# Kernel optimization log

Hardware: AMD Instinct MI355X
Metric: run time of the kernel (lower is better)

## Reference

```python
import jax, jax.numpy as jnp
import numpy as np

WINDOWS = ((0, 4), (2, 6), (4, 8))
N_CLASSES = 64
EPS = 1e-12  # F.normalize eps


def setup_inputs() -> dict:
    key = jax.random.key(0)
    k1, k2 = jax.random.split(key)
    S, Q, T, D = 256, 4096, 8, 1024
    support_features = jax.random.normal(k1, (S, T, D), dtype=jnp.float32)
    target_features = jax.random.normal(k2, (Q, T, D), dtype=jnp.float32)
    support_labels = jnp.arange(S, dtype=jnp.int32) % N_CLASSES  # 4 shots per class, sorted-unique order
    logit_scale = jnp.array(0.0, dtype=jnp.float32)
    fusion_logits = jnp.zeros((3,), dtype=jnp.float32)
    return {
        'support_features': support_features,
        'target_features': target_features,
        'support_labels': support_labels,
        'logit_scale': logit_scale,
        'fusion_logits': fusion_logits,
    }


def _l2norm(x):
    n = jnp.sqrt(jnp.sum(x * x, axis=-1, keepdims=True))
    return x / jnp.maximum(n, EPS)


def _pairwise_dist(query_seq, support_seq):
    # query_seq: [Q, Tq, D], support_seq: [K, Ts, D] -> 1 - cosine sim [Q, K, Tq, Ts]
    sim = jnp.einsum('qtd,ksd->qkts', _l2norm(query_seq), _l2norm(support_seq))
    return 1.0 - sim


def _bi_mhm(dists):
    # dists: [Q, K, Tq, Ts]
    return dists.min(axis=3).sum(axis=2) + dists.min(axis=2).sum(axis=2)


def _segments(features):
    # features: [N, T, D] -> [N, n_windows, D] (mean over each window)
    return jnp.stack([features[:, s:e, :].mean(axis=1) for s, e in WINDOWS], axis=1)


def _prototypes(features, labels):
    # scatter-mean over class labels; features: [S, ...], labels: [S]
    sums = jax.ops.segment_sum(features, labels, num_segments=N_CLASSES)
    counts = jax.ops.segment_sum(jnp.ones((features.shape[0],), features.dtype), labels,
                                 num_segments=N_CLASSES)
    return sums / counts[:, None, None]


def reference(support_features, target_features, support_labels, logit_scale, fusion_logits):
    # global (frame-level) bidirectional min-sum chamfer distance to class prototypes
    support_proto = _prototypes(support_features, support_labels)          # [K, T, D]
    global_dist = _bi_mhm(_pairwise_dist(target_features, support_proto))  # [Q, K]

    # segment-level distances
    support_segments = _segments(support_features)                          # [S, 3, D]
    target_segments = _segments(target_features)                            # [Q, 3, D]
    support_seg_proto = _prototypes(support_segments, support_labels)       # [K, 3, D]
    seg_dist = _pairwise_dist(target_segments, support_seg_proto)           # [Q, K, 3, 3]
    seg_q2s = seg_dist.min(axis=3).sum(axis=2)
    seg_s2q = seg_dist.min(axis=2).sum(axis=2)

    fusion = jax.nn.softmax(fusion_logits)
    fused = (fusion[0] * global_dist + fusion[1] * seg_s2q + fusion[2] * seg_q2s)
    fused = fused * jnp.exp(logit_scale)
    return (-fused, -global_dist, -seg_s2q, -seg_q2s)
```

## Files before the change

### kernel.cpp

```cpp
#include <hip/hip_runtime.h>
#include <stdint.h>

typedef unsigned short u16;
typedef short short8 __attribute__((ext_vector_type(8)));
typedef float floatx4 __attribute__((ext_vector_type(4)));

#define KDIM 1024
#define QN   4096
#define KCLS 64
#define QK   (QN * KCLS)


__device__ __forceinline__ u16 f2bf(float x) {
  union { float f; uint32_t u; } un; un.f = x;
  uint32_t u = un.u;
  u += 0x7FFFu + ((u >> 16) & 1u);
  return (u16)(u >> 16);
}

struct alignas(16) F4 { float x, y, z, w; };
struct alignas(8)  U16x4 { u16 a, b, c, d; };

__device__ __forceinline__ float block_sum(float v) {
  __shared__ float sb[4];
  #pragma unroll
  for (int m = 1; m < 64; m <<= 1) v += __shfl_xor(v, m);
  int tid = threadIdx.x;
  if ((tid & 63) == 0) sb[tid >> 6] = v;
  __syncthreads();
  return sb[0] + sb[1] + sb[2] + sb[3];
}

__device__ __forceinline__ void norm_store(float v0, float v1, float v2, float v3,
                                           u16* __restrict__ dst_row, int tid) {
  float ss = block_sum(v0*v0 + v1*v1 + v2*v2 + v3*v3);
  float inv = 1.0f / fmaxf(sqrtf(ss), 1e-12f);
  U16x4 o; o.a = f2bf(v0*inv); o.b = f2bf(v1*inv); o.c = f2bf(v2*inv); o.d = f2bf(v3*inv);
  *(U16x4*)(dst_row + tid*4) = o;
}


__global__ __launch_bounds__(256) void proto_kernel(const float* __restrict__ S,
                                                    u16* __restrict__ Bg) {
  int b = blockIdx.x, tid = threadIdx.x;
  int k = b >> 3, t = b & 7;
  float v0 = 0.f, v1 = 0.f, v2 = 0.f, v3 = 0.f;
  #pragma unroll
  for (int s = 0; s < 4; ++s) {
    const F4 x = *(const F4*)(S + (size_t)(((s*64 + k)*8 + t))*1024 + tid*4);
    v0 += x.x; v1 += x.y; v2 += x.z; v3 += x.w;
  }
  norm_store(v0*0.25f, v1*0.25f, v2*0.25f, v3*0.25f, Bg + (size_t)b*1024, tid);
}

__global__ __launch_bounds__(256) void segproto_kernel(const float* __restrict__ S,
                                                       u16* __restrict__ Bs) {
  int b = blockIdx.x, tid = threadIdx.x;
  int k = b >> 2, w = b & 3;
  if (w == 3) { U16x4 z; z.a = z.b = z.c = z.d = 0; *(U16x4*)(Bs + (size_t)b*1024 + tid*4) = z; return; }
  int t0 = w * 2;
  float v0 = 0.f, v1 = 0.f, v2 = 0.f, v3 = 0.f;
  #pragma unroll
  for (int s = 0; s < 4; ++s)
    #pragma unroll
    for (int f = 0; f < 4; ++f) {
      const F4 x = *(const F4*)(S + (size_t)(((s*64 + k)*8 + t0 + f))*1024 + tid*4);
      v0 += x.x; v1 += x.y; v2 += x.z; v3 += x.w;
    }
  const float c = 1.0f / 16.0f;
  norm_store(v0*c, v1*c, v2*c, v3*c, Bs + (size_t)b*1024, tid);
}

__global__ __launch_bounds__(256) void tnorm_kernel(const float* __restrict__ T,
                                                    u16* __restrict__ Ag) {
  int b = blockIdx.x, tid = threadIdx.x;
  const F4 x = *(const F4*)(T + (size_t)b*1024 + tid*4);
  norm_store(x.x, x.y, x.z, x.w, Ag + (size_t)b*1024, tid);
}

__global__ __launch_bounds__(256) void tseg_kernel(const float* __restrict__ T,
                                                   u16* __restrict__ As) {
  int b = blockIdx.x, tid = threadIdx.x;
  int q = b >> 2, w = b & 3;
  if (w == 3) { U16x4 z; z.a = z.b = z.c = z.d = 0; *(U16x4*)(As + (size_t)b*1024 + tid*4) = z; return; }
  int t0 = w * 2;
  float v0 = 0.f, v1 = 0.f, v2 = 0.f, v3 = 0.f;
  #pragma unroll
  for (int f = 0; f < 4; ++f) {
    const F4 x = *(const F4*)(T + (size_t)(q*8 + t0 + f)*1024 + tid*4);
    v0 += x.x; v1 += x.y; v2 += x.z; v3 += x.w;
  }
  norm_store(v0*0.25f, v1*0.25f, v2*0.25f, v3*0.25f, As + (size_t)b*1024, tid);
}


__device__ __forceinline__ void load_lds16(const u16* g, u16* l) {
  __builtin_amdgcn_global_load_lds((__attribute__((address_space(1))) void*)(g),
                                   (__attribute__((address_space(3))) void*)(l),
                                   16, 0, 0);
}

template <int MODE>
__global__ __launch_bounds__(256) void gemm_kernel(const u16* __restrict__ A,
                                                   const u16* __restrict__ B,
                                                   float* __restrict__ out_a,
                                                   float* __restrict__ out_b) {
  __shared__ __align__(16) u16 At[128 * 64];
  __shared__ __align__(16) u16 Bt[128 * 64];

  const int tid  = threadIdx.x;
  const int lane = tid & 63;
  const int wave = tid >> 6;
  const int wm = wave >> 1, wn = wave & 1;
  const int rowA0 = blockIdx.y * 128;
  const int rowB0 = blockIdx.x * 128;

  floatx4 acc[4][4] = {};

  const int srow = lane >> 3;
  const int scol = ((lane & 7) ^ srow) * 8;

  for (int kb = 0; kb < KDIM; kb += 64) {
    __syncthreads();
    #pragma unroll
    for (int it = 0; it < 4; ++it) {
      const int c = wave * 4 + it;
      load_lds16(A + (size_t)(rowA0 + c*8 + srow) * KDIM + kb + scol, &At[c * 512]);
      load_lds16(B + (size_t)(rowB0 + c*8 + srow) * KDIM + kb + scol, &Bt[c * 512]);
    }
    __syncthreads();
    #pragma unroll
    for (int kk = 0; kk < 2; ++kk) {
      const int kc0 = kk * 4 + (lane >> 4);
      short8 af[4], bf[4];
      #pragma unroll
      for (int i = 0; i < 4; ++i) {
        const int row = wm*64 + i*16 + (lane & 15);
        af[i] = *(const short8*)&At[row*64 + ((kc0 ^ (row & 7)) * 8)];
        const int col = wn*64 + i*16 + (lane & 15);
        bf[i] = *(const short8*)&Bt[col*64 + ((kc0 ^ (col & 7)) * 8)];
      }
      #pragma unroll
      for (int i = 0; i < 4; ++i)
        #pragma unroll
        for (int j = 0; j < 4; ++j)
          acc[i][j] = __builtin_amdgcn_mfma_f32_16x16x32_bf16(af[i], bf[j], acc[i][j], 0, 0, 0);
    }
  }

  if (MODE == 0) {
    const int qBase = blockIdx.y * 16 + wm * 8;
    const int kBase = blockIdx.x * 16 + wn * 8;
    #pragma unroll
    for (int i = 0; i < 4; ++i) {
      #pragma unroll
      for (int j = 0; j < 4; ++j) {
        floatx4 c = acc[i][j];
        float rs = 0.f;
        #pragma unroll
        for (int r = 0; r < 4; ++r) {
          float x = c[r];
          x = fmaxf(x, __shfl_xor(x, 1));
          x = fmaxf(x, __shfl_xor(x, 2));
          x = fmaxf(x, __shfl_xor(x, 4));
          rs += x;
        }
        rs += __shfl_xor(rs, 16);
        float cm = fmaxf(fmaxf(c[0], c[1]), fmaxf(c[2], c[3]));
        cm = fmaxf(cm, __shfl_xor(cm, 16));
        float cs = cm;
        cs += __shfl_xor(cs, 1);
        cs += __shfl_xor(cs, 2);
        cs += __shfl_xor(cs, 4);
        const float tot = rs + cs - 16.0f;
        if ((lane & 23) == 0) {
          const int a = lane >> 5, bb = (lane >> 3) & 1;
          out_a[(size_t)(qBase + i*2 + a) * KCLS + (kBase + j*2 + bb)] = tot;
        }
      }
    }
  } else {
    const int qBase = blockIdx.y * 32 + wm * 16;
    const int kBase = blockIdx.x * 32 + wn * 16;
    const int cv = lane & 3;
    #pragma unroll
    for (int i = 0; i < 4; ++i) {
      #pragma unroll
      for (int j = 0; j < 4; ++j) {
        floatx4 c = acc[i][j];
        float rsum = 0.f;
        #pragma unroll
        for (int r = 0; r < 3; ++r) {
          float x = (cv == 3) ? -3.0e38f : c[r];
          x = fmaxf(x, __shfl_xor(x, 1));
          x = fmaxf(x, __shfl_xor(x, 2));
          rsum += x;
        }
        float cm = fmaxf(fmaxf(c[0], c[1]), c[2]);
        float y = (cv == 3) ? 0.f : cm;
        y += __shfl_xor(y, 1);
        y += __shfl_xor(y, 2);
        if (cv == 0) {
          const int q = qBase + i*4 + (lane >> 4);
          const int k = kBase + j*4 + ((lane >> 2) & 3);
          out_a[(size_t)q * KCLS + k] = y - 3.0f;
          out_b[(size_t)q * KCLS + k] = rsum - 3.0f;
        }
      }
    }
  }
}

__global__ __launch_bounds__(256) void fuse_kernel(const float* __restrict__ fl,
                                                   const float* __restrict__ ls,
                                                   const float* __restrict__ g,
                                                   const float* __restrict__ s2q,
                                                   const float* __restrict__ q2s,
                                                   float* __restrict__ out) {
  const int i = blockIdx.x * 256 + threadIdx.x;
  const float f0 = fl[0], f1 = fl[1], f2 = fl[2];
  const float m = fmaxf(f0, fmaxf(f1, f2));
  const float e0 = expf(f0 - m), e1 = expf(f1 - m), e2 = expf(f2 - m);
  const float sc = expf(ls[0]) / (e0 + e1 + e2);
  out[i] = sc * (e0 * g[i] + e1 * s2q[i] + e2 * q2s[i]);
}


extern "C" void kernel_launch(void* const* d_in, const int* in_sizes, int n_in,
                              void* d_out, int out_size, void* d_ws, size_t ws_size,
                              hipStream_t stream) {
  (void)in_sizes; (void)n_in; (void)out_size; (void)ws_size;
  const float* S  = (const float*)d_in[0];
  const float* T  = (const float*)d_in[1];
  const float* ls = (const float*)d_in[3];
  const float* fl = (const float*)d_in[4];

  float* outF   = (float*)d_out;
  float* outG   = outF + QK;
  float* outS2Q = outF + 2 * (size_t)QK;
  float* outQ2S = outF + 3 * (size_t)QK;

  u16* Ag = (u16*)d_ws;
  u16* As = Ag + (size_t)32768 * 1024;
  u16* Bg = As + (size_t)16384 * 1024;
  u16* Bs = Bg + (size_t)512 * 1024;

  tnorm_kernel   <<<32768, 256, 0, stream>>>(T, Ag);
  tseg_kernel    <<<16384, 256, 0, stream>>>(T, As);
  proto_kernel   <<<512,   256, 0, stream>>>(S, Bg);
  segproto_kernel<<<256,   256, 0, stream>>>(S, Bs);

  gemm_kernel<0><<<dim3(4, 256), 256, 0, stream>>>(Ag, Bg, outG, outG);
  gemm_kernel<1><<<dim3(2, 128), 256, 0, stream>>>(As, Bs, outS2Q, outQ2S);

  fuse_kernel<<<QK / 256, 256, 0, stream>>>(fl, ls, outG, outS2Q, outQ2S, outF);
}
```

Measured before the change: 318.7 us.

## Fuse preprocessing kernels and fold final fusion into segment GEMM epilogue

Merges the four normalization/segment kernels into two per-row kernels that read each target sample's eight frames once and emit both frame-level and segment-level normalized bf16 rows, with all eleven norms reduced together. Support prototypes are likewise built once per class. The separate fuse kernel is removed, and the segment GEMM epilogue computes the fused output directly by reading the global distance. The aim is to cut redundant global reads of the target tensor and the extra launches and elementwise pass. The trade-offs are more registers in the prep kernels and the segment GEMM depending on the global GEMM having finished writing outG, which stream ordering guarantees.

```diff
diff --git a/kernel.cpp b/kernel.cpp
--- a/kernel.cpp
+++ b/kernel.cpp
@@ -21,76 +21,133 @@
 struct alignas(16) F4 { float x, y, z, w; };
 struct alignas(8)  U16x4 { u16 a, b, c, d; };
 
-__device__ __forceinline__ float block_sum(float v) {
-  __shared__ float sb[4];
-  #pragma unroll
-  for (int m = 1; m < 64; m <<= 1) v += __shfl_xor(v, m);
-  int tid = threadIdx.x;
-  if ((tid & 63) == 0) sb[tid >> 6] = v;
+__device__ __forceinline__ float dot4(const F4& a, const F4& b) {
+  return a.x*b.x + a.y*b.y + a.z*b.z + a.w*b.w;
+}
+
+
+__device__ __forceinline__ void reduce11(float (&ss)[11], float (&tot)[11],
+                                         float (*sb)[12], int lane, int wave) {
+  #pragma unroll
+  for (int v = 0; v < 11; ++v) {
+    float x = ss[v];
+    #pragma unroll
+    for (int m = 1; m < 64; m <<= 1) x += __shfl_xor(x, m);
+    ss[v] = x;
+  }
+  if (lane == 0) {
+    #pragma unroll
+    for (int v = 0; v < 11; ++v) sb[wave][v] = ss[v];
+  }
   __syncthreads();
-  return sb[0] + sb[1] + sb[2] + sb[3];
-}
-
-__device__ __forceinline__ void norm_store(float v0, float v1, float v2, float v3,
-                                           u16* __restrict__ dst_row, int tid) {
-  float ss = block_sum(v0*v0 + v1*v1 + v2*v2 + v3*v3);
-  float inv = 1.0f / fmaxf(sqrtf(ss), 1e-12f);
-  U16x4 o; o.a = f2bf(v0*inv); o.b = f2bf(v1*inv); o.c = f2bf(v2*inv); o.d = f2bf(v3*inv);
-  *(U16x4*)(dst_row + tid*4) = o;
-}
-
-
-__global__ __launch_bounds__(256) void proto_kernel(const float* __restrict__ S,
-                                                    u16* __restrict__ Bg) {
-  int b = blockIdx.x, tid = threadIdx.x;
-  int k = b >> 3, t = b & 7;
-  float v0 = 0.f, v1 = 0.f, v2 = 0.f, v3 = 0.f;
-  #pragma unroll
-  for (int s = 0; s < 4; ++s) {
-    const F4 x = *(const F4*)(S + (size_t)(((s*64 + k)*8 + t))*1024 + tid*4);
-    v0 += x.x; v1 += x.y; v2 += x.z; v3 += x.w;
-  }
-  norm_store(v0*0.25f, v1*0.25f, v2*0.25f, v3*0.25f, Bg + (size_t)b*1024, tid);
-}
-
-__global__ __launch_bounds__(256) void segproto_kernel(const float* __restrict__ S,
-                                                       u16* __restrict__ Bs) {
-  int b = blockIdx.x, tid = threadIdx.x;
-  int k = b >> 2, w = b & 3;
-  if (w == 3) { U16x4 z; z.a = z.b = z.c = z.d = 0; *(U16x4*)(Bs + (size_t)b*1024 + tid*4) = z; return; }
-  int t0 = w * 2;
-  float v0 = 0.f, v1 = 0.f, v2 = 0.f, v3 = 0.f;
+  #pragma unroll
+  for (int v = 0; v < 11; ++v)
+    tot[v] = sb[0][v] + sb[1][v] + sb[2][v] + sb[3][v];
+}
+
+__device__ __forceinline__ float inv_norm(float ss) {
+  return 1.0f / fmaxf(sqrtf(ss), 1e-12f);
+}
+
+__global__ __launch_bounds__(256) void prep_T(const float* __restrict__ T,
+                                              u16* __restrict__ Ag,
+                                              u16* __restrict__ As) {
+  __shared__ float sb[4][12];
+  const int q = blockIdx.x, tid = threadIdx.x;
+  const int lane = tid & 63, wave = tid >> 6;
+
+  F4 x[8];
+  #pragma unroll
+  for (int t = 0; t < 8; ++t)
+    x[t] = *(const F4*)(T + (size_t)(q*8 + t)*1024 + tid*4);
+
+  float ss[11], tot[11];
+  #pragma unroll
+  for (int t = 0; t < 8; ++t) ss[t] = dot4(x[t], x[t]);
+  #pragma unroll
+  for (int w = 0; w < 3; ++w) {
+    F4 y;
+    y.x = (x[2*w].x + x[2*w+1].x + x[2*w+2].x + x[2*w+3].x) * 0.25f;
+    y.y = (x[2*w].y + x[2*w+1].y + x[2*w+2].y + x[2*w+3].y) * 0.25f;
+    y.z = (x[2*w].z + x[2*w+1].z + x[2*w+2].z + x[2*w+3].z) * 0.25f;
+    y.w = (x[2*w].w + x[2*w+1].w + x[2*w+2].w + x[2*w+3].w) * 0.25f;
+    ss[8+w] = dot4(y, y);
+  }
+  reduce11(ss, tot, sb, lane, wave);
+
+  #pragma unroll
+  for (int t = 0; t < 8; ++t) {
+    const float inv = inv_norm(tot[t]);
+    U16x4 o; o.a = f2bf(x[t].x*inv); o.b = f2bf(x[t].y*inv);
+    o.c = f2bf(x[t].z*inv); o.d = f2bf(x[t].w*inv);
+    *(U16x4*)(Ag + (size_t)(q*8 + t)*1024 + tid*4) = o;
+  }
+  #pragma unroll
+  for (int w = 0; w < 3; ++w) {
+    const float inv = inv_norm(tot[8+w]) * 0.25f;
+    F4 y;
+    y.x = (x[2*w].x + x[2*w+1].x + x[2*w+2].x + x[2*w+3].x) * inv;
+    y.y = (x[2*w].y + x[2*w+1].y + x[2*w+2].y + x[2*w+3].y) * inv;
+    y.z = (x[2*w].z + x[2*w+1].z + x[2*w+2].z + x[2*w+3].z) * inv;
+    y.w = (x[2*w].w + x[2*w+1].w + x[2*w+2].w + x[2*w+3].w) * inv;
+    U16x4 o; o.a = f2bf(y.x); o.b = f2bf(y.y); o.c = f2bf(y.z); o.d = f2bf(y.w);
+    *(U16x4*)(As + (size_t)(q*4 + w)*1024 + tid*4) = o;
+  }
+  U16x4 z; z.a = z.b = z.c = z.d = 0;
+  *(U16x4*)(As + (size_t)(q*4 + 3)*1024 + tid*4) = z;
+}
+
+__global__ __launch_bounds__(256) void prep_S(const float* __restrict__ S,
+                                              u16* __restrict__ Bg,
+                                              u16* __restrict__ Bs) {
+  __shared__ float sb[4][12];
+  const int k = blockIdx.x, tid = threadIdx.x;
+  const int lane = tid & 63, wave = tid >> 6;
+
+  F4 p[8];
+  #pragma unroll
+  for (int t = 0; t < 8; ++t) { p[t].x = 0.f; p[t].y = 0.f; p[t].z = 0.f; p[t].w = 0.f; }
   #pragma unroll
   for (int s = 0; s < 4; ++s)
     #pragma unroll
-    for (int f = 0; f < 4; ++f) {
-      const F4 x = *(const F4*)(S + (size_t)(((s*64 + k)*8 + t0 + f))*1024 + tid*4);
-      v0 += x.x; v1 += x.y; v2 += x.z; v3 += x.w;
-    }
-  const float c = 1.0f / 16.0f;
-  norm_store(v0*c, v1*c, v2*c, v3*c, Bs + (size_t)b*1024, tid);
-}
-
-__global__ __launch_bounds__(256) void tnorm_kernel(const float* __restrict__ T,
-                                                    u16* __restrict__ Ag) {
-  int b = blockIdx.x, tid = threadIdx.x;
-  const F4 x = *(const F4*)(T + (size_t)b*1024 + tid*4);
-  norm_store(x.x, x.y, x.z, x.w, Ag + (size_t)b*1024, tid);
-}
-
-__global__ __launch_bounds__(256) void tseg_kernel(const float* __restrict__ T,
-                                                   u16* __restrict__ As) {
-  int b = blockIdx.x, tid = threadIdx.x;
-  int q = b >> 2, w = b & 3;
-  if (w == 3) { U16x4 z; z.a = z.b = z.c = z.d = 0; *(U16x4*)(As + (size_t)b*1024 + tid*4) = z; return; }
-  int t0 = w * 2;
-  float v0 = 0.f, v1 = 0.f, v2 = 0.f, v3 = 0.f;
-  #pragma unroll
-  for (int f = 0; f < 4; ++f) {
-    const F4 x = *(const F4*)(T + (size_t)(q*8 + t0 + f)*1024 + tid*4);
-    v0 += x.x; v1 += x.y; v2 += x.z; v3 += x.w;
-  }
-  norm_store(v0*0.25f, v1*0.25f, v2*0.25f, v3*0.25f, As + (size_t)b*1024, tid);
+    for (int t = 0; t < 8; ++t) {
+      const F4 v = *(const F4*)(S + (size_t)(((s*64 + k)*8 + t))*1024 + tid*4);
+      p[t].x += v.x; p[t].y += v.y; p[t].z += v.z; p[t].w += v.w;
+    }
+  float ss[11], tot[11];
+  #pragma unroll
+  for (int t = 0; t < 8; ++t) ss[t] = dot4(p[t], p[t]) * (0.25f * 0.25f);
+  #pragma unroll
+  for (int w = 0; w < 3; ++w) {
+    F4 y;
+    y.x = (p[2*w].x + p[2*w+1].x + p[2*w+2].x + p[2*w+3].x) * 0.0625f;
+    y.y = (p[2*w].y + p[2*w+1].y + p[2*w+2].y + p[2*w+3].y) * 0.0625f;
+    y.z = (p[2*w].z + p[2*w+1].z + p[2*w+2].z + p[2*w+3].z) * 0.0625f;
+    y.w = (p[2*w].w + p[2*w+1].w + p[2*w+2].w + p[2*w+3].w) * 0.0625f;
+    ss[8+w] = dot4(y, y);
+  }
+  reduce11(ss, tot, sb, lane, wave);
+
+  #pragma unroll
+  for (int t = 0; t < 8; ++t) {
+    const float inv = inv_norm(tot[t]) * 0.25f;
+    U16x4 o; o.a = f2bf(p[t].x*inv); o.b = f2bf(p[t].y*inv);
+    o.c = f2bf(p[t].z*inv); o.d = f2bf(p[t].w*inv);
+    *(U16x4*)(Bg + (size_t)(k*8 + t)*1024 + tid*4) = o;
+  }
+  #pragma unroll
+  for (int w = 0; w < 3; ++w) {
+    const float inv = inv_norm(tot[8+w]) * 0.0625f;
+    F4 y;
+    y.x = (p[2*w].x + p[2*w+1].x + p[2*w+2].x + p[2*w+3].x) * inv;
+    y.y = (p[2*w].y + p[2*w+1].y + p[2*w+2].y + p[2*w+3].y) * inv;
+    y.z = (p[2*w].z + p[2*w+1].z + p[2*w+2].z + p[2*w+3].z) * inv;
+    y.w = (p[2*w].w + p[2*w+1].w + p[2*w+2].w + p[2*w+3].w) * inv;
+    U16x4 o; o.a = f2bf(y.x); o.b = f2bf(y.y); o.c = f2bf(y.z); o.d = f2bf(y.w);
+    *(U16x4*)(Bs + (size_t)(k*4 + w)*1024 + tid*4) = o;
+  }
+  U16x4 z; z.a = z.b = z.c = z.d = 0;
+  *(U16x4*)(Bs + (size_t)(k*4 + 3)*1024 + tid*4) = z;
 }
 
 
@@ -104,7 +161,11 @@
 __global__ __launch_bounds__(256) void gemm_kernel(const u16* __restrict__ A,
                                                    const u16* __restrict__ B,
                                                    float* __restrict__ out_a,
-                                                   float* __restrict__ out_b) {
+                                                   float* __restrict__ out_b,
+                                                   const float* __restrict__ outG,
+                                                   float* __restrict__ out_f,
+                                                   const float* __restrict__ fl,
+                                                   const float* __restrict__ ls) {
   __shared__ __align__(16) u16 At[128 * 64];
   __shared__ __align__(16) u16 Bt[128 * 64];
 
@@ -180,6 +241,10 @@
       }
     }
   } else {
+    const float f0 = fl[0], f1 = fl[1], f2 = fl[2];
+    const float mx = fmaxf(f0, fmaxf(f1, f2));
+    const float e0 = __expf(f0 - mx), e1 = __expf(f1 - mx), e2 = __expf(f2 - mx);
+    const float sc = __expf(ls[0]) / (e0 + e1 + e2);
     const int qBase = blockIdx.y * 32 + wm * 16;
     const int kBase = blockIdx.x * 32 + wn * 16;
     const int cv = lane & 3;
@@ -203,26 +268,16 @@
         if (cv == 0) {
           const int q = qBase + i*4 + (lane >> 4);
           const int k = kBase + j*4 + ((lane >> 2) & 3);
-          out_a[(size_t)q * KCLS + k] = y - 3.0f;
-          out_b[(size_t)q * KCLS + k] = rsum - 3.0f;
+          const size_t idx = (size_t)q * KCLS + k;
+          const float s2q = y - 3.0f;
+          const float q2s = rsum - 3.0f;
+          out_a[idx] = s2q;
+          out_b[idx] = q2s;
+          out_f[idx] = sc * (e0 * outG[idx] + e1 * s2q + e2 * q2s);
         }
       }
     }
   }
-}
-
-__global__ __launch_bounds__(256) void fuse_kernel(const float* __restrict__ fl,
-                                                   const float* __restrict__ ls,
-                                                   const float* __restrict__ g,
-                                                   const float* __restrict__ s2q,
-                                                   const float* __restrict__ q2s,
-                                                   float* __restrict__ out) {
-  const int i = blockIdx.x * 256 + threadIdx.x;
-  const float f0 = fl[0], f1 = fl[1], f2 = fl[2];
-  const float m = fmaxf(f0, fmaxf(f1, f2));
-  const float e0 = expf(f0 - m), e1 = expf(f1 - m), e2 = expf(f2 - m);
-  const float sc = expf(ls[0]) / (e0 + e1 + e2);
-  out[i] = sc * (e0 * g[i] + e1 * s2q[i] + e2 * q2s[i]);
 }
 
 
@@ -245,13 +300,9 @@
   u16* Bg = As + (size_t)16384 * 1024;
   u16* Bs = Bg + (size_t)512 * 1024;
 
-  tnorm_kernel   <<<32768, 256, 0, stream>>>(T, Ag);
-  tseg_kernel    <<<16384, 256, 0, stream>>>(T, As);
-  proto_kernel   <<<512,   256, 0, stream>>>(S, Bg);
-  segproto_kernel<<<256,   256, 0, stream>>>(S, Bs);
-
-  gemm_kernel<0><<<dim3(4, 256), 256, 0, stream>>>(Ag, Bg, outG, outG);
-  gemm_kernel<1><<<dim3(2, 128), 256, 0, stream>>>(As, Bs, outS2Q, outQ2S);
-
-  fuse_kernel<<<QK / 256, 256, 0, stream>>>(fl, ls, outG, outS2Q, outQ2S, outF);
-}
+  prep_T<<<4096, 256, 0, stream>>>(T, Ag, As);
+  prep_S<<<64,   256, 0, stream>>>(S, Bg, Bs);
+
+  gemm_kernel<0><<<dim3(4, 256), 256, 0, stream>>>(Ag, Bg, outG, outG, outG, outF, fl, ls);
+  gemm_kernel<1><<<dim3(2, 128), 256, 0, stream>>>(As, Bs, outS2Q, outQ2S, outG, outF, fl, ls);
+}
```

Result: faster. 300.2 us (-5.8%).
